# Optimization experiments

Hardware: AMD Instinct MI355X
Metric: run time of the kernel (lower is better)

## Reference

```python
import jax, jax.numpy as jnp
import numpy as np

B_SZ, N_IN, N_CTX, UNITS, RANK = 4096, 4096, 512, 4096, 256


def setup_inputs() -> dict:
    key = jax.random.key(0)
    ks = jax.random.split(key, 8)
    inputs = jax.random.normal(ks[0], (B_SZ, N_IN), dtype=jnp.float32)
    context = jax.random.normal(ks[1], (B_SZ, N_CTX), dtype=jnp.float32)
    # Orthogonal-ish init approximated by scaled normals (math-equivalent shapes)
    U = jax.random.normal(ks[2], (N_IN, RANK), dtype=jnp.float32) / np.sqrt(N_IN)
    S = jax.random.uniform(ks[3], (RANK,), dtype=jnp.float32, minval=0.5, maxval=1.5)
    V = jax.random.normal(ks[4], (UNITS, RANK), dtype=jnp.float32) / np.sqrt(UNITS)
    W = jax.random.normal(ks[5], (N_CTX, RANK), dtype=jnp.float32) / np.sqrt(N_CTX)
    B = jnp.zeros((RANK,), dtype=jnp.float32)
    bias = jnp.zeros((UNITS,), dtype=jnp.float32)
    return {"inputs": inputs, "context": context, "U": U, "S": S, "V": V, "W": W, "B": B, "bias": bias}


def reference(inputs, context, U, S, V, W, B, bias):
    # chi[b,r] = sigmoid(context @ W + B)
    chi = jax.nn.sigmoid(context @ W + B)                  # [B, R]
    # Original: kernel[b,n,m] = sum_r U[n,r]*S[r]*chi[b,r]*V[m,r];
    # out[b,m] = sum_n x[b,n]*kernel[b,n,m]. Algebraically equal to:
    t = (inputs @ U) * (S * chi)                           # [B, R]
    out = t @ V.T + bias                                   # first '+ self.bias'
    out = out + bias                                       # 'outputs += self.bias' (use_bias=True)
    return jax.nn.relu(out)
```

## Files before the change

kernel.cpp:

```cpp
#include <hip/hip_runtime.h>

#define B_SZ 4096
#define N_IN 4096
#define N_CTX 512
#define UNITS 4096
#define RANK 256
#define ZSPLIT 16

typedef __attribute__((ext_vector_type(8))) __bf16 bf16x8;
typedef __attribute__((ext_vector_type(4))) float f32x4;
typedef __attribute__((ext_vector_type(8))) unsigned short ushort8;

__device__ __forceinline__ unsigned short f2bf(float f) {
    __bf16 h = (__bf16)f;
    return __builtin_bit_cast(unsigned short, h);
}
__device__ __forceinline__ float bf2f(unsigned short h) {
    return __uint_as_float(((unsigned int)h) << 16);
}
__device__ __forceinline__ void gload_lds16(const unsigned short* g, unsigned short* l) {
    __builtin_amdgcn_global_load_lds(
        (const __attribute__((address_space(1))) unsigned int*)g,
        (__attribute__((address_space(3))) unsigned int*)l, 16, 0, 0);
}
__device__ __forceinline__ bf16x8 ldfrag(const unsigned short* p) {
    ushort8 t = *(const ushort8*)p;
    return __builtin_bit_cast(bf16x8, t);
}

__global__ void prep(const float* __restrict__ U, const float* __restrict__ W,
                     const float* __restrict__ V,
                     unsigned short* __restrict__ UT, unsigned short* __restrict__ WT,
                     unsigned short* __restrict__ Vb) {
    __shared__ unsigned short t[64][66];
    int bid = blockIdx.x, tid = threadIdx.x;
    if (bid < 288) {
        const float* src; unsigned short* dst; int R, C, rb, cb;
        if (bid < 256) { src = U; dst = UT; R = N_IN; C = RANK; rb = (bid & 63) * 64; cb = (bid >> 6) * 64; }
        else { int b = bid - 256; src = W; dst = WT; R = N_CTX; C = RANK; rb = (b & 7) * 64; cb = (b >> 3) * 64; }
        int r = tid >> 4, c4 = (tid & 15) * 4;
        for (int i = 0; i < 4; i++) {
            float4 v = *(const float4*)(src + (size_t)(rb + r + i * 16) * C + cb + c4);
            t[r + i * 16][c4 + 0] = f2bf(v.x);
            t[r + i * 16][c4 + 1] = f2bf(v.y);
            t[r + i * 16][c4 + 2] = f2bf(v.z);
            t[r + i * 16][c4 + 3] = f2bf(v.w);
        }
        __syncthreads();
        int c = tid >> 3, r8 = (tid & 7) * 8;
        for (int j = 0; j < 2; j++) {
            int cc = c + j * 32;
            ushort8 o;
            for (int k = 0; k < 8; k++) o[k] = t[r8 + k][cc];
            *(ushort8*)(dst + (size_t)(cb + cc) * R + rb + r8) = o;
        }
    } else {
        size_t base = (size_t)(bid - 288) * 2048 + (size_t)tid * 8;
        float4 a = *(const float4*)(V + base);
        float4 b = *(const float4*)(V + base + 4);
        ushort8 o = { f2bf(a.x), f2bf(a.y), f2bf(a.z), f2bf(a.w),
                      f2bf(b.x), f2bf(b.y), f2bf(b.z), f2bf(b.w) };
        *(ushort8*)(Vb + base) = o;
    }
}


__launch_bounds__(512, 2)
__global__ void k21(const float* __restrict__ X, const unsigned short* __restrict__ UT,
                    unsigned short* __restrict__ T0p,
                    const float* __restrict__ ctx, const unsigned short* __restrict__ WT,
                    const float* __restrict__ S, const float* __restrict__ Bb,
                    unsigned short* __restrict__ Schi) {
    __shared__ char smem[49152];
    int tid = threadIdx.x, bfull = blockIdx.x;
    int w = tid >> 6, lane = tid & 63;
    int ln15 = lane & 15, quad = lane >> 4;
    if (bfull < 512) {
        int z = bfull >> 5, my = bfull & 31;
        unsigned short* As = (unsigned short*)smem;
        unsigned short* Bs = As + 128 * 64;
        int wr = w >> 2, wc = w & 3;
        int tm = my * 128;
        int kbase = z * (N_IN / ZSPLIT);
        f32x4 acc[4][4] = {};
        int arow = tid >> 2, acs0 = (tid & 3) * 2;
        const float* ag = X + (size_t)(tm + arow) * N_IN + kbase + acs0 * 8;
        unsigned short* al0 = As + arow * 64 + ((acs0 + 0) ^ (arow & 7)) * 8;
        unsigned short* al1 = As + arow * 64 + ((acs0 + 1) ^ (arow & 7)) * 8;
        int bl8 = lane >> 3, bcs = lane & 7;
        int bgc = (bcs ^ bl8) * 8;
        for (int kt = 0; kt < (N_IN / ZSPLIT) / 64; kt++) {
            int k0 = kt * 64;
            for (int c = 0; c < 4; c++) {
                int row = w * 32 + c * 8 + bl8;
                gload_lds16(UT + (size_t)row * N_IN + kbase + k0 + bgc, Bs + row * 64 + bcs * 8);
            }
            {
                float4 v0 = *(const float4*)(ag + k0);
                float4 v1 = *(const float4*)(ag + k0 + 4);
                float4 u0 = *(const float4*)(ag + k0 + 8);
                float4 u1 = *(const float4*)(ag + k0 + 12);
                ushort8 a8 = { f2bf(v0.x), f2bf(v0.y), f2bf(v0.z), f2bf(v0.w),
                               f2bf(v1.x), f2bf(v1.y), f2bf(v1.z), f2bf(v1.w) };
                ushort8 b8 = { f2bf(u0.x), f2bf(u0.y), f2bf(u0.z), f2bf(u0.w),
                               f2bf(u1.x), f2bf(u1.y), f2bf(u1.z), f2bf(u1.w) };
                *(ushort8*)al0 = a8;
                *(ushort8*)al1 = b8;
            }
            __syncthreads();
            for (int kh = 0; kh < 2; kh++) {
                int ch = kh * 4 + quad;
                int sw = (ch ^ (ln15 & 7)) * 8;
                bf16x8 af[4];
                for (int i = 0; i < 4; i++)
                    af[i] = ldfrag(As + (wr * 64 + i * 16 + ln15) * 64 + sw);
                for (int j = 0; j < 4; j++) {
                    bf16x8 b = ldfrag(Bs + (wc * 64 + j * 16 + ln15) * 64 + sw);
                    for (int i = 0; i < 4; i++)
                        acc[i][j] = __builtin_amdgcn_mfma_f32_16x16x32_bf16(af[i], b, acc[i][j], 0, 0, 0);
                }
            }
            __syncthreads();
        }
        unsigned short* P = T0p + (size_t)z * B_SZ * RANK;
        unsigned short* ep = (unsigned short*)smem;
        const int EPW = 280;
        int er = tid >> 3, ec0 = tid & 7;
        for (int h = 0; h < 2; h++) {
            if (wr == h) {
                for (int i = 0; i < 4; i++)
                    for (int j = 0; j < 4; j++)
                        for (int r = 0; r < 4; r++)
                            ep[(i * 16 + quad * 4 + r) * EPW + wc * 64 + j * 16 + ln15] = f2bf(acc[i][j][r]);
            }
            __syncthreads();
            for (int k = 0; k < 4; k++) {
                int chunk = ec0 + 8 * k;
                *(ushort8*)(P + (size_t)(tm + h * 64 + er) * RANK + chunk * 8) =
                    *(const ushort8*)(ep + er * EPW + chunk * 8);
            }
            __syncthreads();
        }
    } else {
        int hh = tid >> 8;
        int sb = (bfull - 512) * 2 + hh;
        int bx = sb & 3, by = sb >> 2;
        int t = tid & 255;
        int lw = t >> 6, llane = t & 63;
        int lln15 = llane & 15, lquad = llane >> 4;
        int wr = lw >> 1, wc = lw & 1;
        unsigned short* base = (unsigned short*)smem + hh * 6144;
        unsigned short* As = base;
        unsigned short* Bs = base + 32 * 64;
        int tm = by * 32, tn = bx * 64;
        f32x4 acc2[2] = {};
        int arow = t >> 3, acs = t & 7;
        const float* ag = ctx + (size_t)(tm + arow) * N_CTX + acs * 8;
        unsigned short* al = As + arow * 64 + (acs ^ (arow & 7)) * 8;
        int bl8 = llane >> 3, bcs = llane & 7;
        int bgc = (bcs ^ bl8) * 8;
        for (int kt = 0; kt < 8; kt++) {
            int k0 = kt * 64;
            for (int c = 0; c < 2; c++) {
                int row = lw * 16 + c * 8 + bl8;
                gload_lds16(WT + (size_t)(tn + row) * N_CTX + k0 + bgc, Bs + row * 64 + bcs * 8);
            }
            {
                float4 v0 = *(const float4*)(ag + k0);
                float4 v1 = *(const float4*)(ag + k0 + 4);
                ushort8 a8 = { f2bf(v0.x), f2bf(v0.y), f2bf(v0.z), f2bf(v0.w),
                               f2bf(v1.x), f2bf(v1.y), f2bf(v1.z), f2bf(v1.w) };
                *(ushort8*)al = a8;
            }
            __syncthreads();
            for (int kh = 0; kh < 2; kh++) {
                int ch = kh * 4 + lquad;
                bf16x8 af = ldfrag(As + (wr * 16 + lln15) * 64 + (ch ^ (lln15 & 7)) * 8);
                for (int j = 0; j < 2; j++) {
                    int row = wc * 32 + j * 16 + lln15;
                    bf16x8 bfr = ldfrag(Bs + row * 64 + (ch ^ (lln15 & 7)) * 8);
                    acc2[j] = __builtin_amdgcn_mfma_f32_16x16x32_bf16(af, bfr, acc2[j], 0, 0, 0);
                }
            }
            __syncthreads();
        }
        for (int j = 0; j < 2; j++) {
            int col = tn + wc * 32 + j * 16 + lln15;
            float sv = S[col], bv = Bb[col];
            for (int r = 0; r < 4; r++) {
                int row = tm + wr * 16 + lquad * 4 + r;
                float x = acc2[j][r] + bv;
                float chi = sv / (1.f + __expf(-x));
                Schi[(size_t)row * RANK + col] = f2bf(chi);
            }
        }
    }
}

__global__ void e_red(const unsigned short* __restrict__ T0p, const unsigned short* __restrict__ Schi,
                      unsigned short* __restrict__ T) {
    int i = blockIdx.x * 256 + threadIdx.x;
    const size_t stride = (size_t)B_SZ * RANK;
    float a[8] = {};
    for (int z = 0; z < ZSPLIT; z++) {
        ushort8 p = *(const ushort8*)(T0p + z * stride + (size_t)i * 8);
        for (int k = 0; k < 8; k++) a[k] += bf2f(p[k]);
    }
    ushort8 s = *(const ushort8*)(Schi + (size_t)i * 8);
    ushort8 o;
    for (int k = 0; k < 8; k++) o[k] = f2bf(a[k] * bf2f(s[k]));
    *(ushort8*)(T + (size_t)i * 8) = o;
}

__launch_bounds__(512, 2)
__global__ void k3_out(const unsigned short* __restrict__ T, const unsigned short* __restrict__ Vb,
                       const float* __restrict__ bias, float* __restrict__ out) {
    __shared__ char smem[66560];
    unsigned short* As = (unsigned short*)smem;
    unsigned short* Bs = As + 128 * 64;
    int tid = threadIdx.x, w = tid >> 6, lane = tid & 63;
    int ln15 = lane & 15, quad = lane >> 4;
    int wr = w >> 2, wc = w & 3;
    int tn = blockIdx.x * 256, tm = blockIdx.y * 128;
    f32x4 acc[4][4] = {};
    int bl8 = lane >> 3, bcs = lane & 7;
    int bgc = (bcs ^ bl8) * 8;
    for (int kt = 0; kt < RANK / 64; kt++) {
        int k0 = kt * 64;
        for (int c = 0; c < 2; c++) {
            int row = w * 16 + c * 8 + bl8;
            gload_lds16(T + (size_t)(tm + row) * RANK + k0 + bgc, As + row * 64 + bcs * 8);
        }
        for (int c = 0; c < 4; c++) {
            int row = w * 32 + c * 8 + bl8;
            gload_lds16(Vb + (size_t)(tn + row) * RANK + k0 + bgc, Bs + row * 64 + bcs * 8);
        }
        __syncthreads();
        for (int kh = 0; kh < 2; kh++) {
            int ch = kh * 4 + quad;
            int sw = (ch ^ (ln15 & 7)) * 8;
            bf16x8 af[4];
            for (int i = 0; i < 4; i++)
                af[i] = ldfrag(As + (wr * 64 + i * 16 + ln15) * 64 + sw);
            for (int j = 0; j < 4; j++) {
                bf16x8 b = ldfrag(Bs + (wc * 64 + j * 16 + ln15) * 64 + sw);
                for (int i = 0; i < 4; i++)
                    acc[i][j] = __builtin_amdgcn_mfma_f32_16x16x32_bf16(af[i], b, acc[i][j], 0, 0, 0);
            }
        }
        __syncthreads();
    }
    float* ep = (float*)smem;
    const int EPW = 260;
    int er = tid >> 3, ec0 = tid & 7;
    for (int h = 0; h < 2; h++) {
        if (wr == h) {
            for (int j = 0; j < 4; j++) {
                int col = wc * 64 + j * 16 + ln15;
                float bv = 2.f * bias[tn + col];
                for (int i = 0; i < 4; i++)
                    for (int r = 0; r < 4; r++)
                        ep[(i * 16 + quad * 4 + r) * EPW + col] = fmaxf(acc[i][j][r] + bv, 0.f);
            }
        }
        __syncthreads();
        for (int k = 0; k < 8; k++) {
            int chunk = ec0 + 8 * k;
            *(float4*)(out + (size_t)(tm + h * 64 + er) * UNITS + tn + chunk * 4) =
                *(const float4*)(ep + er * EPW + chunk * 4);
        }
        __syncthreads();
    }
}

extern "C" void kernel_launch(void* const* d_in, const int* in_sizes, int n_in,
                              void* d_out, int out_size, void* d_ws, size_t ws_size,
                              hipStream_t stream) {
    (void)in_sizes; (void)n_in; (void)out_size; (void)ws_size;
    const float* inputs  = (const float*)d_in[0];
    const float* context = (const float*)d_in[1];
    const float* U       = (const float*)d_in[2];
    const float* S       = (const float*)d_in[3];
    const float* V       = (const float*)d_in[4];
    const float* W       = (const float*)d_in[5];
    const float* Bb      = (const float*)d_in[6];
    const float* bias    = (const float*)d_in[7];
    float* out = (float*)d_out;

    char* ws = (char*)d_ws;
    size_t o = 0;
    unsigned short* UT   = (unsigned short*)(ws + o); o += (size_t)RANK * N_IN * 2;
    unsigned short* WT   = (unsigned short*)(ws + o); o += (size_t)RANK * N_CTX * 2;
    unsigned short* Vb   = (unsigned short*)(ws + o); o += (size_t)UNITS * RANK * 2;
    unsigned short* Schi = (unsigned short*)(ws + o); o += (size_t)B_SZ * RANK * 2;
    unsigned short* T    = (unsigned short*)(ws + o); o += (size_t)B_SZ * RANK * 2;
    unsigned short* T0p  = (unsigned short*)(ws + o); o += (size_t)ZSPLIT * B_SZ * RANK * 2;

    prep<<<800, 256, 0, stream>>>(U, W, V, UT, WT, Vb);
    k21<<<768, 512, 0, stream>>>(inputs, UT, T0p, context, WT, S, Bb, Schi);
    e_red<<<(B_SZ * RANK) / (256 * 8), 256, 0, stream>>>(T0p, Schi, T);
    k3_out<<<dim3(UNITS / 256, B_SZ / 128), 512, 0, stream>>>(T, Vb, bias, out);
}
```

Baseline: 175.0 us.

## Keep V tile resident in LDS and stream T row blocks with double buffering

The output GEMM kernel now loads a full 128x256 slice of V into LDS once per block and loops over eight 64-row slices of T. Each T slice is prefetched into a second buffer while the current one is being computed. The grid shrinks to 256 persistent-style blocks, each using 160 KB of LDS at one block per CU. This removes repeated V reloads and the K-loop barriers, but each block now does less MFMA work per output tile and there are fewer waves available to hide latency.

```diff
diff --git a/kernel.cpp b/kernel.cpp
--- a/kernel.cpp
+++ b/kernel.cpp
@@ -212,65 +212,82 @@
     *(ushort8*)(T + (size_t)i * 8) = o;
 }
 
-__launch_bounds__(512, 2)
+__launch_bounds__(512, 1)
 __global__ void k3_out(const unsigned short* __restrict__ T, const unsigned short* __restrict__ Vb,
                        const float* __restrict__ bias, float* __restrict__ out) {
-    __shared__ char smem[66560];
-    unsigned short* As = (unsigned short*)smem;
-    unsigned short* Bs = As + 128 * 64;
+    __shared__ char smem[163840];
+    unsigned short* Bs = (unsigned short*)smem;
+    unsigned short* A0 = (unsigned short*)(smem + 65536);
+    unsigned short* A1 = A0 + 64 * 256;
+    float* ep = (float*)(smem + 131072);
     int tid = threadIdx.x, w = tid >> 6, lane = tid & 63;
     int ln15 = lane & 15, quad = lane >> 4;
     int wr = w >> 2, wc = w & 3;
-    int tn = blockIdx.x * 256, tm = blockIdx.y * 128;
-    f32x4 acc[4][4] = {};
-    int bl8 = lane >> 3, bcs = lane & 7;
-    int bgc = (bcs ^ bl8) * 8;
-    for (int kt = 0; kt < RANK / 64; kt++) {
-        int k0 = kt * 64;
-        for (int c = 0; c < 2; c++) {
-            int row = w * 16 + c * 8 + bl8;
-            gload_lds16(T + (size_t)(tm + row) * RANK + k0 + bgc, As + row * 64 + bcs * 8);
-        }
-        for (int c = 0; c < 4; c++) {
-            int row = w * 32 + c * 8 + bl8;
-            gload_lds16(Vb + (size_t)(tn + row) * RANK + k0 + bgc, Bs + row * 64 + bcs * 8);
-        }
-        __syncthreads();
-        for (int kh = 0; kh < 2; kh++) {
-            int ch = kh * 4 + quad;
-            int sw = (ch ^ (ln15 & 7)) * 8;
-            bf16x8 af[4];
-            for (int i = 0; i < 4; i++)
-                af[i] = ldfrag(As + (wr * 64 + i * 16 + ln15) * 64 + sw);
-            for (int j = 0; j < 4; j++) {
-                bf16x8 b = ldfrag(Bs + (wc * 64 + j * 16 + ln15) * 64 + sw);
-                for (int i = 0; i < 4; i++)
-                    acc[i][j] = __builtin_amdgcn_mfma_f32_16x16x32_bf16(af[i], b, acc[i][j], 0, 0, 0);
-            }
-        }
-        __syncthreads();
-    }
-    float* ep = (float*)smem;
-    const int EPW = 260;
-    int er = tid >> 3, ec0 = tid & 7;
-    for (int h = 0; h < 2; h++) {
-        if (wr == h) {
-            for (int j = 0; j < 4; j++) {
-                int col = wc * 64 + j * 16 + ln15;
-                float bv = 2.f * bias[tn + col];
-                for (int i = 0; i < 4; i++)
-                    for (int r = 0; r < 4; r++)
-                        ep[(i * 16 + quad * 4 + r) * EPW + col] = fmaxf(acc[i][j][r] + bv, 0.f);
-            }
-        }
-        __syncthreads();
-        for (int k = 0; k < 8; k++) {
-            int chunk = ec0 + 8 * k;
-            *(float4*)(out + (size_t)(tm + h * 64 + er) * UNITS + tn + chunk * 4) =
-                *(const float4*)(ep + er * EPW + chunk * 4);
-        }
-        __syncthreads();
-    }
+    int tn = blockIdx.x * 128;
+    int tmg = blockIdx.y * 512;
+    int lr2 = lane >> 5, lc16 = lane & 31;
+
+    for (int i = 0; i < 8; i++) {
+        int row = (w * 8 + i) * 2 + lr2;
+        int g = (lc16 & 24) | ((lc16 & 7) ^ (row & 7));
+        gload_lds16(Vb + (size_t)(tn + row) * RANK + g * 8, Bs + row * 256 + lc16 * 8);
+    }
+#define STAGE_A3(buf, step) do { \
+    for (int i = 0; i < 4; i++) { \
+        int row = (w * 4 + i) * 2 + lr2; \
+        int g = (lc16 & 24) | ((lc16 & 7) ^ (row & 7)); \
+        gload_lds16(T + (size_t)(tmg + (step) * 64 + row) * RANK + g * 8, \
+                    (buf) + row * 256 + lc16 * 8); \
+    } } while (0)
+    STAGE_A3(A0, 0);
+    float bv0 = 2.f * bias[tn + wc * 32 + ln15];
+    float bv1 = 2.f * bias[tn + wc * 32 + 16 + ln15];
+    unsigned short* cur = A0;
+    unsigned short* nxt = A1;
+    for (int t = 0; t < 8; t++) {
+        STAGE_A3(nxt, (t + 1) & 7);
+        asm volatile("s_waitcnt vmcnt(4)" ::: "memory");
+        __builtin_amdgcn_s_barrier();
+        __builtin_amdgcn_sched_barrier(0);
+        f32x4 acc[2][2] = {};
+        for (int kh = 0; kh < 8; kh++) {
+            int c = kh * 4 + quad;
+            bf16x8 af[2], bf[2];
+            for (int i = 0; i < 2; i++) {
+                int row = wr * 32 + i * 16 + ln15;
+                int c16 = (c & 24) | ((c & 7) ^ (row & 7));
+                af[i] = ldfrag(cur + row * 256 + c16 * 8);
+            }
+            for (int j = 0; j < 2; j++) {
+                int row = wc * 32 + j * 16 + ln15;
+                int c16 = (c & 24) | ((c & 7) ^ (row & 7));
+                bf[j] = ldfrag(Bs + row * 256 + c16 * 8);
+            }
+            for (int i = 0; i < 2; i++)
+                for (int j = 0; j < 2; j++)
+                    acc[i][j] = __builtin_amdgcn_mfma_f32_16x16x32_bf16(af[i], bf[j], acc[i][j], 0, 0, 0);
+        }
+        for (int i = 0; i < 2; i++)
+            for (int j = 0; j < 2; j++) {
+                float bv = j ? bv1 : bv0;
+                for (int r = 0; r < 4; r++)
+                    ep[(wr * 32 + i * 16 + quad * 4 + r) * 128 + wc * 32 + j * 16 + ln15] =
+                        fmaxf(acc[i][j][r] + bv, 0.f);
+            }
+        asm volatile("s_waitcnt lgkmcnt(0)" ::: "memory");
+        __builtin_amdgcn_s_barrier();
+        __builtin_amdgcn_sched_barrier(0);
+        {
+            int er = tid >> 3, ec = tid & 7;
+            size_t orow = (size_t)(tmg + t * 64 + er) * UNITS + tn;
+            for (int k = 0; k < 4; k++)
+                *(float4*)(out + orow + (ec + k * 8) * 4) =
+                    *(const float4*)(ep + er * 128 + (ec + k * 8) * 4);
+        }
+        __builtin_amdgcn_s_barrier();
+        unsigned short* tmp = cur; cur = nxt; nxt = tmp;
+    }
+#undef STAGE_A3
 }
 
 extern "C" void kernel_launch(void* const* d_in, const int* in_sizes, int n_in,
@@ -299,5 +316,5 @@
     prep<<<800, 256, 0, stream>>>(U, W, V, UT, WT, Vb);
     k21<<<768, 512, 0, stream>>>(inputs, UT, T0p, context, WT, S, Bb, Schi);
     e_red<<<(B_SZ * RANK) / (256 * 8), 256, 0, stream>>>(T0p, Schi, T);
-    k3_out<<<dim3(UNITS / 256, B_SZ / 128), 512, 0, stream>>>(T, Vb, bias, out);
-}
+    k3_out<<<dim3(32, 8), 512, 0, stream>>>(T, Vb, bias, out);
+}
```

After: 176.5 us. Within noise of the previous version (+0.9%).
